# Performance work log

Measured on AMD Instinct MI355X. Metric: run time of the kernel, lower is better.

Reference implementation:

```python
import jax, jax.numpy as jnp
import numpy as np

N_SPK, N_UTT, D = 512, 64, 1024
EPS = 1e-6  # matches tf.math.l2_normalize default epsilon guard


def _l2norm(x, axis=-1):
    return x / jnp.sqrt(jnp.maximum(jnp.sum(x * x, axis=axis, keepdims=True), EPS))


def setup_inputs() -> dict:
    key = jax.random.key(0)
    k1, _ = jax.random.split(key)
    inputs = jax.random.normal(k1, (N_SPK, N_UTT, D), dtype=jnp.float32)
    w = jnp.asarray(10.0, dtype=jnp.float32)
    b = jnp.asarray(-5.0, dtype=jnp.float32)
    return {"inputs": inputs, "w": w, "b": b}


def reference(inputs, w, b):
    N, M, _ = inputs.shape
    # speaker centroids: mean over utterances -> [N, D]
    centroids = jnp.mean(inputs, axis=1)
    # utterance (exclusion) centroids: mean of the other M-1 utterances -> [N, M, D]
    ut_centroids = (jnp.sum(inputs, axis=1, keepdims=True) - inputs) / (M - 1)

    e = _l2norm(inputs)          # [N, M, D]
    c = _l2norm(centroids)       # [N, D]
    uc = _l2norm(ut_centroids)   # [N, M, D]

    # cosine sim of every utterance vs every speaker centroid -> [N, M, K]
    cos_all = jnp.einsum('nmd,kd->nmk', e, c)
    # same-speaker entries use the self-exclusion centroid
    cos_self = jnp.sum(e * uc, axis=-1)  # [N, M]
    eye = jnp.eye(N, dtype=inputs.dtype)[:, None, :]  # [N, 1, N]
    cos_sim = cos_all * (1.0 - eye) + cos_self[:, :, None] * eye

    sim = w * cos_sim + b  # [N, M, N]
    # softmax contrastive loss: -S_{j,i,j} + logsumexp_k S_{j,i,k}, summed
    lse = jax.nn.logsumexp(sim, axis=-1)            # [N, M]
    pos = jnp.einsum('nmn->nm', sim)                # diagonal along speaker axes
    loss = jnp.sum(lse - pos)
    return loss
```

## Files before the change

kernel.cpp:

```cpp
#include <hip/hip_runtime.h>
#include <stdint.h>

#define N_SPK 512
#define N_UTT 64
#define DIM   1024
#define NROWS (N_SPK * N_UTT)
#define EPS   1e-6f

#define BM 128
#define BN 128
#define BK 32
#define KTILES (DIM / BK)

typedef __attribute__((ext_vector_type(8))) short short8;
typedef __attribute__((ext_vector_type(4))) float f32x4;

__device__ __forceinline__ uint16_t f2bf(float f) {
    union { float f; uint32_t i; } un; un.f = f;
    uint32_t x = un.i;
    return (uint16_t)((x + 0x7fffu + ((x >> 16) & 1u)) >> 16);
}

__global__ __launch_bounds__(256) void prep_centroid(
    const float* __restrict__ x, uint16_t* __restrict__ xb,
    uint16_t* __restrict__ cmat, float* __restrict__ xxg,
    float* __restrict__ ssqg)
{
    const int n    = blockIdx.x;
    const int tid  = threadIdx.x;
    const int lane = tid & 63;
    const int w    = tid >> 6;

    const float* xn  = x  + (size_t)n * N_UTT * DIM;
    uint16_t*    xbn = xb + (size_t)n * N_UTT * DIM;

    float Sp[16];
    #pragma unroll
    for (int j = 0; j < 16; ++j) Sp[j] = 0.f;

    #pragma unroll 1
    for (int o = 0; o < 4; ++o) {
        const int m0 = w * 16 + o * 4;

        float4 v[16];
        #pragma unroll
        for (int i = 0; i < 4; ++i)
            #pragma unroll
            for (int j = 0; j < 4; ++j)
                v[i * 4 + j] = *(const float4*)(xn + (size_t)(m0 + i) * DIM + j * 256 + lane * 4);

        float xx[4] = {0.f, 0.f, 0.f, 0.f};
        #pragma unroll
        for (int i = 0; i < 4; ++i) {
            #pragma unroll
            for (int j = 0; j < 4; ++j) {
                const float4 q = v[i * 4 + j];
                xx[i] += q.x * q.x + q.y * q.y + q.z * q.z + q.w * q.w;
                Sp[j * 4 + 0] += q.x; Sp[j * 4 + 1] += q.y;
                Sp[j * 4 + 2] += q.z; Sp[j * 4 + 3] += q.w;
                ushort4 ov;
                ov.x = f2bf(q.x); ov.y = f2bf(q.y); ov.z = f2bf(q.z); ov.w = f2bf(q.w);
                *(ushort4*)(xbn + (size_t)(m0 + i) * DIM + j * 256 + lane * 4) = ov;
            }
        }

        #pragma unroll
        for (int i = 0; i < 4; ++i) {
            float t = xx[i];
            #pragma unroll
            for (int off = 1; off < 64; off <<= 1) t += __shfl_xor(t, off);
            if (lane == 0) xxg[n * N_UTT + m0 + i] = t;
        }
    }

    __shared__ float Sh[4][DIM];
    #pragma unroll
    for (int j = 0; j < 4; ++j)
        *(float4*)&Sh[w][j * 256 + lane * 4] =
            make_float4(Sp[j * 4], Sp[j * 4 + 1], Sp[j * 4 + 2], Sp[j * 4 + 3]);
    __syncthreads();

    const int d0 = tid * 4;
    float4 S  = *(const float4*)&Sh[0][d0];
    const float4 b1 = *(const float4*)&Sh[1][d0];
    const float4 b2 = *(const float4*)&Sh[2][d0];
    const float4 b3 = *(const float4*)&Sh[3][d0];
    S.x += b1.x + b2.x + b3.x; S.y += b1.y + b2.y + b3.y;
    S.z += b1.z + b2.z + b3.z; S.w += b1.w + b2.w + b3.w;

    float css = S.x * S.x + S.y * S.y + S.z * S.z + S.w * S.w;
    #pragma unroll
    for (int off = 1; off < 64; off <<= 1) css += __shfl_xor(css, off);
    __shared__ float red[4];
    if ((tid & 63) == 0) red[tid >> 6] = css;
    __syncthreads();
    const float ssq = red[0] + red[1] + red[2] + red[3];

    const float scale = rsqrtf(fmaxf(ssq * (1.0f / 4096.f), EPS)) * (1.0f / 64.f);
    ushort4 oc;
    oc.x = f2bf(S.x * scale); oc.y = f2bf(S.y * scale);
    oc.z = f2bf(S.z * scale); oc.w = f2bf(S.w * scale);
    *(ushort4*)(cmat + (size_t)n * DIM + d0) = oc;
    if (tid == 0) ssqg[n] = ssq;
}

__global__ __launch_bounds__(256) void gemm_lse_kernel(
    const uint16_t* __restrict__ xb, const uint16_t* __restrict__ cmat,
    const float* __restrict__ xxg, const float* __restrict__ ssqg,
    const float* __restrict__ wp, const float* __restrict__ bp,
    float* __restrict__ sumexp4, float* __restrict__ pos)
{
    __shared__ uint16_t Asm[BM * BK];
    __shared__ uint16_t Bsm[BN * BK];
    __shared__ float    SeLDS[BM];

    const int tid   = threadIdx.x;
    const int lane  = tid & 63;
    const int wid   = tid >> 6;
    const int waveM = wid >> 1;
    const int waveN = wid & 1;

    const int bid = blockIdx.x;
    const int rt  = (bid & 7) | ((bid >> 5) << 3);
    const int ct  = (bid >> 3) & 3;

    const int rowBase = rt * BM;
    const int colBase = ct * BN;

    const uint16_t* gA[2];
    const uint16_t* gB[2];
    #pragma unroll
    for (int i = 0; i < 2; ++i) {
        const int s    = i * 256 + tid;
        const int srow = s >> 2;
        const int kc   = (s & 3) ^ ((srow >> 1) & 3);
        gA[i] = xb   + (size_t)(rowBase + srow) * DIM + kc * 8;
        gB[i] = cmat + (size_t)(colBase + srow) * DIM + kc * 8;
    }

    f32x4 acc[4][4];
    #pragma unroll
    for (int i = 0; i < 4; ++i)
        #pragma unroll
        for (int j = 0; j < 4; ++j)
            acc[i][j] = (f32x4){0.f, 0.f, 0.f, 0.f};

    const int cL  = lane & 15;
    const int q   = lane >> 4;
    const int key = (cL >> 1) & 3;
    const int kcs = q ^ key;

    for (int kt = 0; kt < KTILES; ++kt) {
        __syncthreads();
        const int ko = kt * BK;
        #pragma unroll
        for (int i = 0; i < 2; ++i) {
            __builtin_amdgcn_global_load_lds(
                (const __attribute__((address_space(1))) void*)(gA[i] + ko),
                (__attribute__((address_space(3))) void*)(&Asm[(i * 256 + wid * 64) * 8]),
                16, 0, 0);
            __builtin_amdgcn_global_load_lds(
                (const __attribute__((address_space(1))) void*)(gB[i] + ko),
                (__attribute__((address_space(3))) void*)(&Bsm[(i * 256 + wid * 64) * 8]),
                16, 0, 0);
        }
        __syncthreads();

        short8 a[4], b[4];
        #pragma unroll
        for (int bi = 0; bi < 4; ++bi)
            a[bi] = *(const short8*)&Asm[(waveM * 64 + bi * 16 + cL) * BK + kcs * 8];
        #pragma unroll
        for (int bj = 0; bj < 4; ++bj)
            b[bj] = *(const short8*)&Bsm[(waveN * 64 + bj * 16 + cL) * BK + kcs * 8];

        #pragma unroll
        for (int bi = 0; bi < 4; ++bi)
            #pragma unroll
            for (int bj = 0; bj < 4; ++bj)
                acc[bi][bj] = __builtin_amdgcn_mfma_f32_16x16x32_bf16(
                    a[bi], b[bj], acc[bi][bj], 0, 0, 0);
    }

    const float wv = wp[0], bv = bp[0];
    float srow[16];
    #pragma unroll
    for (int bi = 0; bi < 4; ++bi) {
        #pragma unroll
        for (int r = 0; r < 4; ++r) {
            const int R     = rowBase + waveM * 64 + bi * 16 + q * 4 + r;
            const float xxv = xxg[R];
            const float rn  = rsqrtf(fmaxf(xxv, EPS));
            const int nrow  = R >> 6;
            float s = 0.f;
            #pragma unroll
            for (int bj = 0; bj < 4; ++bj) {
                const int col = colBase + waveN * 64 + bj * 16 + cL;
                const float dot = acc[bi][bj][r];
                float sim;
                if (col == nrow) {
                    const float ssqv = ssqg[nrow];
                    const float xs   = dot * sqrtf(ssqv);
                    const float d2   = ssqv - 2.f * xs + xxv;
                    const float cs   = ((xs - xxv) * (1.f / 63.f)) * rn *
                                       rsqrtf(fmaxf(d2 * (1.f / 3969.f), EPS));
                    sim = wv * cs + bv;
                    pos[R] = sim;
                } else {
                    sim = wv * (dot * rn) + bv;
                }
                s += __expf(sim);
            }
            #pragma unroll
            for (int off = 1; off < 16; off <<= 1) s += __shfl_xor(s, off);
            srow[bi * 4 + r] = s;
        }
    }

    if (waveN == 1 && cL == 0) {
        #pragma unroll
        for (int bi = 0; bi < 4; ++bi)
            #pragma unroll
            for (int r = 0; r < 4; ++r)
                SeLDS[waveM * 64 + bi * 16 + q * 4 + r] = srow[bi * 4 + r];
    }
    __syncthreads();
    if (waveN == 0 && cL == 0) {
        #pragma unroll
        for (int bi = 0; bi < 4; ++bi)
            #pragma unroll
            for (int r = 0; r < 4; ++r) {
                const int lr = waveM * 64 + bi * 16 + q * 4 + r;
                sumexp4[(size_t)ct * NROWS + rowBase + lr] = srow[bi * 4 + r] + SeLDS[lr];
            }
    }
}

__global__ __launch_bounds__(256) void finalize_part(
    const float* __restrict__ pos, const float* __restrict__ se4,
    float* __restrict__ partial)
{
    const int tid = threadIdx.x;
    const int r   = blockIdx.x * 256 + tid;
    const float s = se4[r] + se4[NROWS + r] + se4[2 * NROWS + r] + se4[3 * NROWS + r];
    float acc = __logf(s) - pos[r];
    #pragma unroll
    for (int off = 1; off < 64; off <<= 1) acc += __shfl_xor(acc, off);
    __shared__ float red[4];
    if ((tid & 63) == 0) red[tid >> 6] = acc;
    __syncthreads();
    if (tid == 0) partial[blockIdx.x] = red[0] + red[1] + red[2] + red[3];
}

__global__ __launch_bounds__(128) void finalize_sum(
    const float* __restrict__ partial, float* __restrict__ out)
{
    const int tid = threadIdx.x;
    float t = partial[tid];
    #pragma unroll
    for (int off = 1; off < 64; off <<= 1) t += __shfl_xor(t, off);
    __shared__ float red[2];
    if ((tid & 63) == 0) red[tid >> 6] = t;
    __syncthreads();
    if (tid == 0) out[0] = red[0] + red[1];
}

extern "C" void kernel_launch(void* const* d_in, const int* in_sizes, int n_in,
                              void* d_out, int out_size, void* d_ws, size_t ws_size,
                              hipStream_t stream)
{
    const float* x  = (const float*)d_in[0];
    const float* wp = (const float*)d_in[1];
    const float* bp = (const float*)d_in[2];
    float* out = (float*)d_out;

    char* ws = (char*)d_ws;
    size_t off = 0;
    uint16_t* xb      = (uint16_t*)(ws + off); off += (size_t)NROWS * DIM * 2;
    uint16_t* cmat    = (uint16_t*)(ws + off); off += (size_t)N_SPK * DIM * 2;
    float*    xxg     = (float*)(ws + off);    off += (size_t)NROWS * 4;
    float*    pos     = (float*)(ws + off);    off += (size_t)NROWS * 4;
    float*    sumexp4 = (float*)(ws + off);    off += (size_t)4 * NROWS * 4;
    float*    ssqg    = (float*)(ws + off);    off += (size_t)N_SPK * 4;
    float*    partial = (float*)(ws + off);    off += (size_t)128 * 4;

    prep_centroid<<<N_SPK, 256, 0, stream>>>(x, xb, cmat, xxg, ssqg);
    gemm_lse_kernel<<<(NROWS / BM) * (N_SPK / BN), 256, 0, stream>>>(
        xb, cmat, xxg, ssqg, wp, bp, sumexp4, pos);
    finalize_part<<<NROWS / 256, 256, 0, stream>>>(pos, sumexp4, partial);
    finalize_sum<<<1, 128, 0, stream>>>(partial, out);
}
```

Baseline: 260.4 us.

## Enlarge GEMM tile to 256x256 with double-buffered LDS and 8 waves

The fused GEMM+sum-exp kernel moves from 128x128 tiles with 4 waves to 256x256 tiles with 8 waves, each wave computing a 128x64 sub-tile. The LDS tile loads are double-buffered so the next K-slice is fetched while MFMAs run on the current one, which also drops one barrier per iteration. The column split shrinks from 4 to 2 partial sum-exp buffers, and the reduction now goes through shared memory. The costs are more accumulator registers per thread, 64KB of LDS per block, and only 256 blocks, which may leave the GPU under-occupied.

```diff
diff --git a/kernel.cpp b/kernel.cpp
--- a/kernel.cpp
+++ b/kernel.cpp
@@ -7,10 +7,10 @@
 #define NROWS (N_SPK * N_UTT)
 #define EPS   1e-6f
 
-#define BM 128
-#define BN 128
-#define BK 32
-#define KTILES (DIM / BK)
+#define BM2 256
+#define BN2 256
+#define BK2 32
+#define KT2 (DIM / BK2)
 
 typedef __attribute__((ext_vector_type(8))) short short8;
 typedef __attribute__((ext_vector_type(4))) float f32x4;
@@ -54,12 +54,12 @@
         for (int i = 0; i < 4; ++i) {
             #pragma unroll
             for (int j = 0; j < 4; ++j) {
-                const float4 q = v[i * 4 + j];
-                xx[i] += q.x * q.x + q.y * q.y + q.z * q.z + q.w * q.w;
-                Sp[j * 4 + 0] += q.x; Sp[j * 4 + 1] += q.y;
-                Sp[j * 4 + 2] += q.z; Sp[j * 4 + 3] += q.w;
+                const float4 qv = v[i * 4 + j];
+                xx[i] += qv.x * qv.x + qv.y * qv.y + qv.z * qv.z + qv.w * qv.w;
+                Sp[j * 4 + 0] += qv.x; Sp[j * 4 + 1] += qv.y;
+                Sp[j * 4 + 2] += qv.z; Sp[j * 4 + 3] += qv.w;
                 ushort4 ov;
-                ov.x = f2bf(q.x); ov.y = f2bf(q.y); ov.z = f2bf(q.z); ov.w = f2bf(q.w);
+                ov.x = f2bf(qv.x); ov.y = f2bf(qv.y); ov.z = f2bf(qv.z); ov.w = f2bf(qv.w);
                 *(ushort4*)(xbn + (size_t)(m0 + i) * DIM + j * 256 + lane * 4) = ov;
             }
         }
@@ -104,91 +104,110 @@
     if (tid == 0) ssqg[n] = ssq;
 }
 
-__global__ __launch_bounds__(256) void gemm_lse_kernel(
+__global__ __launch_bounds__(512, 2) void gemm_lse_kernel(
     const uint16_t* __restrict__ xb, const uint16_t* __restrict__ cmat,
     const float* __restrict__ xxg, const float* __restrict__ ssqg,
     const float* __restrict__ wp, const float* __restrict__ bp,
-    float* __restrict__ sumexp4, float* __restrict__ pos)
-{
-    __shared__ uint16_t Asm[BM * BK];
-    __shared__ uint16_t Bsm[BN * BK];
-    __shared__ float    SeLDS[BM];
+    float* __restrict__ sumexp2, float* __restrict__ pos)
+{
+    __shared__ char smem[65536];
+    uint16_t* As = (uint16_t*)smem;
+    uint16_t* Bs = (uint16_t*)(smem + 32768);
+    float*    Se = (float*)smem;
 
     const int tid   = threadIdx.x;
     const int lane  = tid & 63;
     const int wid   = tid >> 6;
-    const int waveM = wid >> 1;
-    const int waveN = wid & 1;
+    const int waveM = wid >> 2;
+    const int waveN = wid & 3;
 
     const int bid = blockIdx.x;
-    const int rt  = (bid & 7) | ((bid >> 5) << 3);
-    const int ct  = (bid >> 3) & 3;
-
-    const int rowBase = rt * BM;
-    const int colBase = ct * BN;
-
-    const uint16_t* gA[2];
-    const uint16_t* gB[2];
+    const int rt  = bid & 127;
+    const int ct  = bid >> 7;
+
+    const int rowBase = rt * BM2;
+    const int colBase = ct * BN2;
+
+    const uint16_t* gAp[2];
+    const uint16_t* gBp[2];
+    int ldso[2];
     #pragma unroll
     for (int i = 0; i < 2; ++i) {
-        const int s    = i * 256 + tid;
+        const int s    = i * 512 + tid;
         const int srow = s >> 2;
-        const int kc   = (s & 3) ^ ((srow >> 1) & 3);
-        gA[i] = xb   + (size_t)(rowBase + srow) * DIM + kc * 8;
-        gB[i] = cmat + (size_t)(colBase + srow) * DIM + kc * 8;
-    }
-
-    f32x4 acc[4][4];
-    #pragma unroll
-    for (int i = 0; i < 4; ++i)
+        const int kc   = (s & 3) ^ (srow & 3);
+        gAp[i]  = xb   + (size_t)(rowBase + srow) * DIM + kc * 8;
+        gBp[i]  = cmat + (size_t)(colBase + srow) * DIM + kc * 8;
+        ldso[i] = s * 16;
+    }
+
+#define STAGE(buf, ko)                                                          \
+    {                                                                           \
+        _Pragma("unroll")                                                       \
+        for (int i_ = 0; i_ < 2; ++i_) {                                        \
+            __builtin_amdgcn_global_load_lds(                                   \
+                (const __attribute__((address_space(1))) void*)(gAp[i_] + (ko)),\
+                (__attribute__((address_space(3))) void*)(smem + (buf) * 16384 + ldso[i_]), \
+                16, 0, 0);                                                      \
+            __builtin_amdgcn_global_load_lds(                                   \
+                (const __attribute__((address_space(1))) void*)(gBp[i_] + (ko)),\
+                (__attribute__((address_space(3))) void*)(smem + 32768 + (buf) * 16384 + ldso[i_]), \
+                16, 0, 0);                                                      \
+        }                                                                       \
+    }
+
+    f32x4 acc[8][4];
+    #pragma unroll
+    for (int i = 0; i < 8; ++i)
         #pragma unroll
         for (int j = 0; j < 4; ++j)
             acc[i][j] = (f32x4){0.f, 0.f, 0.f, 0.f};
 
-    const int cL  = lane & 15;
-    const int q   = lane >> 4;
-    const int key = (cL >> 1) & 3;
-    const int kcs = q ^ key;
-
-    for (int kt = 0; kt < KTILES; ++kt) {
-        __syncthreads();
-        const int ko = kt * BK;
-        #pragma unroll
-        for (int i = 0; i < 2; ++i) {
-            __builtin_amdgcn_global_load_lds(
-                (const __attribute__((address_space(1))) void*)(gA[i] + ko),
-                (__attribute__((address_space(3))) void*)(&Asm[(i * 256 + wid * 64) * 8]),
-                16, 0, 0);
-            __builtin_amdgcn_global_load_lds(
-                (const __attribute__((address_space(1))) void*)(gB[i] + ko),
-                (__attribute__((address_space(3))) void*)(&Bsm[(i * 256 + wid * 64) * 8]),
-                16, 0, 0);
-        }
-        __syncthreads();
-
-        short8 a[4], b[4];
-        #pragma unroll
-        for (int bi = 0; bi < 4; ++bi)
-            a[bi] = *(const short8*)&Asm[(waveM * 64 + bi * 16 + cL) * BK + kcs * 8];
-        #pragma unroll
-        for (int bj = 0; bj < 4; ++bj)
-            b[bj] = *(const short8*)&Bsm[(waveN * 64 + bj * 16 + cL) * BK + kcs * 8];
-
-        #pragma unroll
-        for (int bi = 0; bi < 4; ++bi)
+    const int cL = lane & 15;
+    const int q  = lane >> 4;
+
+    STAGE(0, 0);
+    __syncthreads();
+
+    int cur = 0;
+    for (int kt = 0; kt < KT2; ++kt) {
+        if (kt + 1 < KT2) STAGE(cur ^ 1, (kt + 1) * BK2);
+
+        const uint16_t* Ab = As + cur * (256 * 32);
+        const uint16_t* Bb = Bs + cur * (256 * 32);
+
+        short8 a[8], b[4];
+        #pragma unroll
+        for (int bi = 0; bi < 8; ++bi) {
+            const int row = waveM * 128 + bi * 16 + cL;
+            const int ch  = q ^ (row & 3);
+            a[bi] = *(const short8*)&Ab[row * 32 + ch * 8];
+        }
+        #pragma unroll
+        for (int bj = 0; bj < 4; ++bj) {
+            const int row = waveN * 64 + bj * 16 + cL;
+            const int ch  = q ^ (row & 3);
+            b[bj] = *(const short8*)&Bb[row * 32 + ch * 8];
+        }
+
+        #pragma unroll
+        for (int bi = 0; bi < 8; ++bi)
             #pragma unroll
             for (int bj = 0; bj < 4; ++bj)
                 acc[bi][bj] = __builtin_amdgcn_mfma_f32_16x16x32_bf16(
                     a[bi], b[bj], acc[bi][bj], 0, 0, 0);
-    }
+
+        __syncthreads();
+        cur ^= 1;
+    }
+#undef STAGE
 
     const float wv = wp[0], bv = bp[0];
-    float srow[16];
-    #pragma unroll
-    for (int bi = 0; bi < 4; ++bi) {
+    #pragma unroll
+    for (int bi = 0; bi < 8; ++bi) {
         #pragma unroll
         for (int r = 0; r < 4; ++r) {
-            const int R     = rowBase + waveM * 64 + bi * 16 + q * 4 + r;
+            const int R     = rowBase + waveM * 128 + bi * 16 + q * 4 + r;
             const float xxv = xxg[R];
             const float rn  = rsqrtf(fmaxf(xxv, EPS));
             const int nrow  = R >> 6;
@@ -213,36 +232,24 @@
             }
             #pragma unroll
             for (int off = 1; off < 16; off <<= 1) s += __shfl_xor(s, off);
-            srow[bi * 4 + r] = s;
-        }
-    }
-
-    if (waveN == 1 && cL == 0) {
-        #pragma unroll
-        for (int bi = 0; bi < 4; ++bi)
-            #pragma unroll
-            for (int r = 0; r < 4; ++r)
-                SeLDS[waveM * 64 + bi * 16 + q * 4 + r] = srow[bi * 4 + r];
-    }
-    __syncthreads();
-    if (waveN == 0 && cL == 0) {
-        #pragma unroll
-        for (int bi = 0; bi < 4; ++bi)
-            #pragma unroll
-            for (int r = 0; r < 4; ++r) {
-                const int lr = waveM * 64 + bi * 16 + q * 4 + r;
-                sumexp4[(size_t)ct * NROWS + rowBase + lr] = srow[bi * 4 + r] + SeLDS[lr];
-            }
+            if (cL == 0)
+                Se[waveN * 256 + waveM * 128 + bi * 16 + q * 4 + r] = s;
+        }
+    }
+    __syncthreads();
+    if (tid < 256) {
+        const float t = Se[tid] + Se[256 + tid] + Se[512 + tid] + Se[768 + tid];
+        sumexp2[(size_t)ct * NROWS + rowBase + tid] = t;
     }
 }
 
 __global__ __launch_bounds__(256) void finalize_part(
-    const float* __restrict__ pos, const float* __restrict__ se4,
+    const float* __restrict__ pos, const float* __restrict__ se2,
     float* __restrict__ partial)
 {
     const int tid = threadIdx.x;
     const int r   = blockIdx.x * 256 + tid;
-    const float s = se4[r] + se4[NROWS + r] + se4[2 * NROWS + r] + se4[3 * NROWS + r];
+    const float s = se2[r] + se2[NROWS + r];
     float acc = __logf(s) - pos[r];
     #pragma unroll
     for (int off = 1; off < 64; off <<= 1) acc += __shfl_xor(acc, off);
@@ -280,13 +287,13 @@
     uint16_t* cmat    = (uint16_t*)(ws + off); off += (size_t)N_SPK * DIM * 2;
     float*    xxg     = (float*)(ws + off);    off += (size_t)NROWS * 4;
     float*    pos     = (float*)(ws + off);    off += (size_t)NROWS * 4;
-    float*    sumexp4 = (float*)(ws + off);    off += (size_t)4 * NROWS * 4;
+    float*    sumexp2 = (float*)(ws + off);    off += (size_t)2 * NROWS * 4;
     float*    ssqg    = (float*)(ws + off);    off += (size_t)N_SPK * 4;
     float*    partial = (float*)(ws + off);    off += (size_t)128 * 4;
 
     prep_centroid<<<N_SPK, 256, 0, stream>>>(x, xb, cmat, xxg, ssqg);
-    gemm_lse_kernel<<<(NROWS / BM) * (N_SPK / BN), 256, 0, stream>>>(
-        xb, cmat, xxg, ssqg, wp, bp, sumexp4, pos);
-    finalize_part<<<NROWS / 256, 256, 0, stream>>>(pos, sumexp4, partial);
+    gemm_lse_kernel<<<(NROWS / BM2) * (N_SPK / BN2), 512, 0, stream>>>(
+        xb, cmat, xxg, ssqg, wp, bp, sumexp2, pos);
+    finalize_part<<<NROWS / 256, 256, 0, stream>>>(pos, sumexp2, partial);
     finalize_sum<<<1, 128, 0, stream>>>(partial, out);
 }
```

Measured after the change: 253.5 us. 2.7% less time.
